# Kernel optimization log

Measured on AMD Instinct MI355X. Metric: run time of the kernel, lower is better.

## Reference

```python
import jax, jax.numpy as jnp
import numpy as np

N = 2048
GRID = 125
G3 = GRID ** 3
DX = 10.0 / GRID
INV_DX = 1.0 / DX
DENSITY = 1000.0
DT0 = 0.0417

_OFF = np.array([[i, j, k] for i in range(3) for j in range(3) for k in range(3)], dtype=np.int32)  # 27 stencil offsets


def setup_inputs() -> dict:
    key = jax.random.key(0)
    k1, k2, k3, k4 = jax.random.split(key, 4)
    bs, T = 2, 16
    x = jax.random.uniform(k1, (bs, T, N, 3), dtype=jnp.float32)
    vol = jax.random.uniform(k2, (bs, N), dtype=jnp.float32)
    F = jax.random.normal(k3, (bs, T, N, 3, 3), dtype=jnp.float32)
    C = jax.random.normal(k4, (bs, T, N, 3, 3), dtype=jnp.float32)
    return {"x": x, "vol": vol, "F": F, "C": C, "frame_interval": 2, "norm_fac": 5}


def reference(x, vol, F, C, frame_interval, norm_fac):
    if norm_fac > 0:
        x = x * 2 + norm_fac
    dT = DT0 * frame_interval
    bs, T = x.shape[0], x.shape[1]
    start_t = 1 if frame_interval == 1 else 0
    end_t = T - 2
    M = bs * (end_t - start_t)

    px = x[:, start_t:end_t].reshape(M, N, 3)
    pv = ((x[:, start_t + 2:end_t + 2] - x[:, start_t:end_t]) / (2 * dT)).reshape(M, N, 3)
    pF = F[:, start_t:end_t].reshape(M, N, 3, 3)
    pFn = F[:, start_t + 1:end_t + 1].reshape(M, N, 3, 3)
    pC = C[:, start_t:end_t].reshape(M, N, 3, 3)
    mass = DENSITY * jnp.repeat(vol[:, None], end_t - start_t, axis=1).reshape(M, N)  # [M,N]

    gp = px * INV_DX
    base = (gp - 0.5).astype(jnp.int32)            # positions are positive -> trunc == floor
    fx = gp - base                                  # [M,N,3]
    # quadratic B-spline weights, axis-major: w[..., axis, offset]
    w = jnp.stack([0.5 * (1.5 - fx) ** 2, 0.75 - (fx - 1) ** 2, 0.5 * (fx - 0.5) ** 2], axis=-1)
    dw = jnp.stack([fx - 1.5, -2 * (fx - 1), fx - 0.5], axis=-1)

    off = jnp.asarray(_OFF)                         # [27,3]
    wi = w[:, :, 0, off[:, 0]]; wj = w[:, :, 1, off[:, 1]]; wk = w[:, :, 2, off[:, 2]]
    dwi = dw[:, :, 0, off[:, 0]]; dwj = dw[:, :, 1, off[:, 1]]; dwk = dw[:, :, 2, off[:, 2]]
    weight = wi * wj * wk                           # [M,N,27]
    dweight = jnp.stack([dwi * wj * wk, wi * dwj * wk, wi * wj * dwk], axis=-1) * INV_DX  # [M,N,27,3]

    node = base[:, :, None, :] + off[None, None]    # [M,N,27,3]
    flat = (node[..., 0] * GRID + node[..., 1]) * GRID + node[..., 2]  # [M,N,27]

    dpos = (off[None, None].astype(fx.dtype) - fx[:, :, None, :]) * DX  # [M,N,27,3]
    vel = pv[:, :, None, :] + jnp.einsum('mnab,mnob->mnoa', pC, dpos)   # APIC velocity
    mw = mass[:, :, None] * weight                  # [M,N,27]
    v_in = mw[..., None] * vel                      # [M,N,27,3]

    midx = jnp.arange(M)[:, None, None]
    grid_v = jnp.zeros((M, G3, 3), x.dtype).at[midx, flat].add(v_in)   # P2G momentum scatter
    grid_m = jnp.zeros((M, G3), x.dtype).at[midx, flat].add(mw)        # P2G mass scatter
    grid_m = jnp.where(grid_m > 1e-15, grid_m, jnp.ones_like(grid_m))
    grid_v = grid_v / grid_m[..., None]

    gv = grid_v[midx, flat]                          # G2P gather [M,N,27,3]
    new_F = jnp.einsum('mnoa,mnob->mnab', gv, dweight)  # velocity gradient
    I3 = jnp.eye(3, dtype=x.dtype)
    F_pred = jnp.einsum('mnab,mnbc->mnac', I3 + new_F * dT, pF)
    return jnp.mean(jnp.abs(F_pred - pFn)) * (end_t - start_t)
```

## Files before the change

### kernel.cpp

```cpp
#include <hip/hip_runtime.h>

constexpr float DT0      = 0.0417f;
constexpr float DENSITY_ = 1000.0f;
constexpr float DXF      = 10.0f / 125.0f;
constexpr float INV_DXF  = 12.5f;

constexpr int DIM  = 32;
constexpr int DIM2 = DIM * DIM;
constexpr int DIM3 = DIM * DIM * DIM;

constexpr float MSC = 1.0f / 16.0f;

typedef _Float16 f16x2 __attribute__((ext_vector_type(2)));

__device__ __forceinline__ void lds_pk_fadd(f16x2* addr, f16x2 v) {
#if __has_builtin(__builtin_amdgcn_ds_atomic_fadd_v2f16)
    (void)__builtin_amdgcn_ds_atomic_fadd_v2f16(
        (__attribute__((address_space(3))) f16x2*)addr, v);
#else
    unsigned int* ua = (unsigned int*)addr;
    union { f16x2 h; unsigned int u; } oldv, newv, cur;
    cur.u = __atomic_load_n(ua, __ATOMIC_RELAXED);
    do {
        oldv.u = cur.u;
        newv.h = oldv.h + v;
        cur.u  = atomicCAS(ua, oldv.u, newv.u);
    } while (cur.u != oldv.u);
#endif
}

__device__ __forceinline__ f16x2 pk_f16(float lo, float hi) {
#if __has_builtin(__builtin_amdgcn_cvt_pkrtz)
    return __builtin_bit_cast(f16x2, __builtin_amdgcn_cvt_pkrtz(lo, hi));
#else
    f16x2 v; v.x = (_Float16)lo; v.y = (_Float16)hi; return v;
#endif
}

__device__ __forceinline__ int window_min(int nf) {
    int b = 0;
    if (nf > 0) {
        b = (int)(12.5f * (float)nf - 0.5f) - 2;
        if (b < 0) b = 0;
    }
    return b;
}

__global__ __launch_bounds__(1024)
void p2g_kernel(const float* __restrict__ x,
                const float* __restrict__ vol,
                const float* __restrict__ C,
                const int* __restrict__ fi_p,
                const int* __restrict__ nf_p,
                float* __restrict__ grid,
                int bs, int T, int Np)
{
    __shared__ f16x2 pl[4][DIM2 * 2];

    const int fi = fi_p[0], nf = nf_p[0];
    const int start_t = (fi == 1) ? 1 : 0;
    const int TS = (T - 2) - start_t;
    const int M  = bs * TS;

    const int m   = blockIdx.x >> 5;
    const int p   = blockIdx.x & (DIM - 1);
    const int tid = threadIdx.x;
    const int q   = tid >> 8;
    const int lt  = tid & 255;

    f16x2* plf = &pl[0][0];
    f16x2 hz; hz.x = (_Float16)0.0f; hz.y = (_Float16)0.0f;
    for (int i = tid; i < 4 * DIM2 * 2; i += 1024) plf[i] = hz;
    __syncthreads();

    if (m < M) {
        const int b = m / TS;
        const int t = (m - b * TS) + start_t;
        const int bmin = window_min(nf);
        const float dT = DT0 * (float)fi;
        const float inv2dT = 1.0f / (2.0f * dT);
        const float nff = (float)nf;

        const float* x0s = x + (((size_t)b * T + t)     * Np) * 3;
        const float* x2s = x + (((size_t)b * T + t + 2) * Np) * 3;
        const float* Cs  = C + (((size_t)b * T + t)     * Np) * 9;
        const float* vs  = vol + (size_t)b * Np;

        f16x2* myp = pl[q];
        const int nbeg = q * (Np >> 2);
        const int nend = nbeg + (Np >> 2);

        for (int n = nbeg + lt; n < nend; n += 256) {
            float a0 = x0s[3 * n];
            if (nf > 0) a0 = a0 * 2.0f + nff;
            const float gp0 = a0 * INV_DXF;
            const int b0 = (int)(gp0 - 0.5f);
            const int l0 = b0 - bmin;
            const int i  = p - l0;
            if ((unsigned)i > 2u) continue;

            float a1 = x0s[3 * n + 1], a2 = x0s[3 * n + 2];
            float c0 = x2s[3 * n], c1 = x2s[3 * n + 1], c2 = x2s[3 * n + 2];
            if (nf > 0) {
                a1 = a1 * 2.0f + nff; a2 = a2 * 2.0f + nff;
                c0 = c0 * 2.0f + nff; c1 = c1 * 2.0f + nff; c2 = c2 * 2.0f + nff;
            }
            const float pv0 = (c0 - a0) * inv2dT;
            const float pv1 = (c1 - a1) * inv2dT;
            const float pv2 = (c2 - a2) * inv2dT;
            const float mass = DENSITY_ * vs[n];
            float Cm[9];
#pragma unroll
            for (int r = 0; r < 9; ++r) Cm[r] = Cs[9 * n + r];

            const float fx0 = gp0 - (float)b0;
            const float gp1 = a1 * INV_DXF;
            const int   b1  = (int)(gp1 - 0.5f);
            const float fx1 = gp1 - (float)b1;
            const float gp2 = a2 * INV_DXF;
            const int   b2  = (int)(gp2 - 0.5f);
            const float fx2 = gp2 - (float)b2;
            const int l1 = b1 - bmin, l2 = b2 - bmin;

            const float wi = (i == 0) ? 0.5f * (1.5f - fx0) * (1.5f - fx0)
                           : (i == 1) ? 0.75f - (fx0 - 1.0f) * (fx0 - 1.0f)
                                      : 0.5f * (fx0 - 0.5f) * (fx0 - 0.5f);
            const float wim = mass * wi * MSC;

            float w1a[3], w2a[3];
            w1a[0] = 0.5f * (1.5f - fx1) * (1.5f - fx1);
            w1a[1] = 0.75f - (fx1 - 1.0f) * (fx1 - 1.0f);
            w1a[2] = 0.5f * (fx1 - 0.5f) * (fx1 - 0.5f);
            w2a[0] = 0.5f * (1.5f - fx2) * (1.5f - fx2);
            w2a[1] = 0.75f - (fx2 - 1.0f) * (fx2 - 1.0f);
            w2a[2] = 0.5f * (fx2 - 0.5f) * (fx2 - 0.5f);

            const float dpx  = ((float)i - fx0) * DXF;
            const float dpy0 = (-fx1) * DXF;
            const float dpz0 = (-fx2) * DXF;
            float vjx = pv0 + Cm[0]*dpx + Cm[1]*dpy0 + Cm[2]*dpz0;
            float vjy = pv1 + Cm[3]*dpx + Cm[4]*dpy0 + Cm[5]*dpz0;
            float vjz = pv2 + Cm[6]*dpx + Cm[7]*dpy0 + Cm[8]*dpz0;
            const float djx = Cm[1] * DXF, djy = Cm[4] * DXF, djz = Cm[7] * DXF;
            const float dkx = Cm[2] * DXF, dky = Cm[5] * DXF, dkz = Cm[8] * DXF;

            if (l1 >= 0 && l1 <= DIM - 3 && l2 >= 0 && l2 <= DIM - 3) {
                int rowc = (l1 * DIM + l2) * 2;
#pragma unroll
                for (int j = 0; j < 3; ++j) {
                    const float wijm = wim * w1a[j];
                    float vx = vjx, vy = vjy, vz = vjz;
                    int cc = rowc;
#pragma unroll
                    for (int k = 0; k < 3; ++k) {
                        const float mw = wijm * w2a[k];
                        lds_pk_fadd(&myp[cc + 0], pk_f16(mw * vx, mw * vy));
                        lds_pk_fadd(&myp[cc + 1], pk_f16(mw * vz, mw));
                        vx += dkx; vy += dky; vz += dkz;
                        cc += 2;
                    }
                    vjx += djx; vjy += djy; vjz += djz;
                    rowc += DIM * 2;
                }
            } else {
#pragma unroll
                for (int j = 0; j < 3; ++j) {
                    const int lj = min(max(l1 + j, 0), DIM - 1);
                    const float wijm = wim * w1a[j];
                    float vx = vjx, vy = vjy, vz = vjz;
#pragma unroll
                    for (int k = 0; k < 3; ++k) {
                        const int lk = min(max(l2 + k, 0), DIM - 1);
                        const float mw = wijm * w2a[k];
                        const int cc = (lj * DIM + lk) * 2;
                        lds_pk_fadd(&myp[cc + 0], pk_f16(mw * vx, mw * vy));
                        lds_pk_fadd(&myp[cc + 1], pk_f16(mw * vz, mw));
                        vx += dkx; vy += dky; vz += dkz;
                    }
                    vjx += djx; vjy += djy; vjz += djz;
                }
            }
        }
    }
    __syncthreads();

    if (m < M) {
        float4* dst = (float4*)(grid + ((size_t)m * DIM + p) * DIM2 * 4);
        for (int cell = tid; cell < DIM2; cell += 1024) {
            float mx = 0.f, my = 0.f, mz = 0.f, gm = 0.f;
#pragma unroll
            for (int cp = 0; cp < 4; ++cp) {
                const f16x2 s0 = pl[cp][cell * 2 + 0];
                const f16x2 s1 = pl[cp][cell * 2 + 1];
                mx += (float)s0.x; my += (float)s0.y;
                mz += (float)s1.x; gm += (float)s1.y;
            }
            const float inv = (gm > 1e-12f) ? 1.0f / gm : 0.0f;
            dst[cell] = make_float4(mx * inv, my * inv, mz * inv, 0.0f);
        }
    }
}

__global__ __launch_bounds__(256)
void g2p_loss_kernel(const float* __restrict__ x,
                     const float* __restrict__ F,
                     const int* __restrict__ fi_p,
                     const int* __restrict__ nf_p,
                     const float* __restrict__ grid,
                     float* __restrict__ partials,
                     int bs, int T, int Np)
{
    const int fi = fi_p[0], nf = nf_p[0];
    const int start_t = (fi == 1) ? 1 : 0;
    const int TS = (T - 2) - start_t;
    const int M  = bs * TS;
    const float dT = DT0 * (float)fi;

    const int gid = blockIdx.x * blockDim.x + threadIdx.x;
    const int pid = gid >> 2;
    const int q   = gid & 3;
    float s = 0.0f;

    if (pid < M * Np) {
        const int m = pid / Np;
        const int n = pid - m * Np;
        const int b = m / TS;
        const int t = (m - b * TS) + start_t;
        const float nff = (float)nf;

        const float* x0 = x + (((size_t)b * T + t) * Np + n) * 3;
        float px[3];
#pragma unroll
        for (int d = 0; d < 3; ++d) {
            float a0 = x0[d];
            if (nf > 0) a0 = a0 * 2.0f + nff;
            px[d] = a0;
        }

        const int bmin = window_min(nf);
        int   base[3];
        float fx[3], w[3][3], dw[3][3];
#pragma unroll
        for (int d = 0; d < 3; ++d) {
            const float gp = px[d] * INV_DXF;
            base[d] = (int)(gp - 0.5f);
            fx[d]   = gp - (float)base[d];
            w[d][0] = 0.5f * (1.5f - fx[d]) * (1.5f - fx[d]);
            w[d][1] = 0.75f - (fx[d] - 1.0f) * (fx[d] - 1.0f);
            w[d][2] = 0.5f * (fx[d] - 0.5f) * (fx[d] - 0.5f);
            dw[d][0] = fx[d] - 1.5f;
            dw[d][1] = -2.0f * (fx[d] - 1.0f);
            dw[d][2] = fx[d] - 0.5f;
        }

        const float* gbase = grid + (size_t)m * DIM3 * 4;
        float nF[9] = {0,0,0,0,0,0,0,0,0};
#pragma unroll
        for (int o = q; o < 27; o += 4) {
            const int i = o / 9, j = (o / 3) % 3, k = o % 3;
            const int li = min(max(base[0] + i - bmin, 0), DIM - 1);
            const int lj = min(max(base[1] + j - bmin, 0), DIM - 1);
            const int lk = min(max(base[2] + k - bmin, 0), DIM - 1);
            const float4 g = *(const float4*)(gbase +
                ((size_t)((li * DIM + lj) * DIM + lk)) * 4);
            const float gx = g.x, gy = g.y, gz = g.z;
            const float dwx = dw[0][i] *  w[1][j] *  w[2][k] * INV_DXF;
            const float dwy =  w[0][i] * dw[1][j] *  w[2][k] * INV_DXF;
            const float dwz =  w[0][i] *  w[1][j] * dw[2][k] * INV_DXF;
            nF[0] += gx * dwx; nF[1] += gx * dwy; nF[2] += gx * dwz;
            nF[3] += gy * dwx; nF[4] += gy * dwy; nF[5] += gy * dwz;
            nF[6] += gz * dwx; nF[7] += gz * dwy; nF[8] += gz * dwz;
        }
#pragma unroll
        for (int d = 1; d < 4; d <<= 1) {
#pragma unroll
            for (int r = 0; r < 9; ++r) nF[r] += __shfl_xor(nF[r], d, 64);
        }

        if (q == 0) {
            const float* pF  = F + (((size_t)b * T + t)     * Np + n) * 9;
            const float* pFn = F + (((size_t)b * T + t + 1) * Np + n) * 9;
            float Fm[9], Fn[9];
#pragma unroll
            for (int i = 0; i < 9; ++i) { Fm[i] = pF[i]; Fn[i] = pFn[i]; }
#pragma unroll
            for (int a = 0; a < 3; ++a) {
#pragma unroll
                for (int c = 0; c < 3; ++c) {
                    const float fp = Fm[a * 3 + c] + dT *
                        (nF[a * 3 + 0] * Fm[0 + c] +
                         nF[a * 3 + 1] * Fm[3 + c] +
                         nF[a * 3 + 2] * Fm[6 + c]);
                    s += fabsf(fp - Fn[a * 3 + c]);
                }
            }
            s *= (float)TS / ((float)M * (float)Np * 9.0f);
        }
    }

#pragma unroll
    for (int o = 32; o > 0; o >>= 1) s += __shfl_down(s, o, 64);
    __shared__ float wsum[4];
    const int lane = threadIdx.x & 63;
    const int wid  = threadIdx.x >> 6;
    if (lane == 0) wsum[wid] = s;
    __syncthreads();
    if (threadIdx.x == 0)
        partials[blockIdx.x] = wsum[0] + wsum[1] + wsum[2] + wsum[3];
}

__global__ __launch_bounds__(256)
void reduce_kernel(const float* __restrict__ partials, int n,
                   float* __restrict__ out)
{
    float s = 0.0f;
    for (int i = threadIdx.x; i < n; i += 256) s += partials[i];
#pragma unroll
    for (int o = 32; o > 0; o >>= 1) s += __shfl_down(s, o, 64);
    __shared__ float wsum[4];
    const int lane = threadIdx.x & 63;
    const int wid  = threadIdx.x >> 6;
    if (lane == 0) wsum[wid] = s;
    __syncthreads();
    if (threadIdx.x == 0) out[0] = wsum[0] + wsum[1] + wsum[2] + wsum[3];
}

extern "C" void kernel_launch(void* const* d_in, const int* in_sizes, int n_in,
                              void* d_out, int out_size, void* d_ws, size_t ws_size,
                              hipStream_t stream) {
    const float* x   = (const float*)d_in[0];
    const float* vol = (const float*)d_in[1];
    const float* F   = (const float*)d_in[2];
    const float* C   = (const float*)d_in[3];
    const int*   fi  = (const int*)d_in[4];
    const int*   nf  = (const int*)d_in[5];

    const int Np = 2048;
    const int bs = in_sizes[1] / Np;
    const int T  = in_sizes[0] / (bs * Np * 3);
    const int MMAX = bs * (T - 2);

    float* grid = (float*)d_ws;
    const size_t grid_f = (size_t)MMAX * DIM3 * 4;
    float* partials = grid + grid_f;

    p2g_kernel<<<MMAX * DIM, 1024, 0, stream>>>(x, vol, C, fi, nf,
                                                grid, bs, T, Np);

    const int nthreads = MMAX * Np * 4;
    const int nblocks  = (nthreads + 255) / 256;
    g2p_loss_kernel<<<nblocks, 256, 0, stream>>>(
        x, F, fi, nf, grid, partials, bs, T, Np);

    reduce_kernel<<<1, 256, 0, stream>>>(partials, nblocks, (float*)d_out);
}
```

Baseline: 110.7 us.

## Compact matching particles into LDS queue before P2G scatter; split final F error across lanes

In P2G, every thread first tests whether its particle touches this block's x-slab and appends matching indices to a shared-memory queue through wave ballot and atomic counter. All 1024 threads then process the compacted queue, so the expensive scatter work is spread evenly instead of leaving most lanes idle inside divergent waves. In G2P, the final F_pred error computation is split across the four sub-lanes rather than done only by q==0. The cost is an extra barrier and LDS queue space, and the 11-bit particle index encoding assumes Np <= 2048.

```diff
diff --git a/kernel.cpp b/kernel.cpp
--- a/kernel.cpp
+++ b/kernel.cpp
@@ -56,6 +56,8 @@
                 int bs, int T, int Np)
 {
     __shared__ f16x2 pl[4][DIM2 * 2];
+    __shared__ unsigned short queue[2048];
+    __shared__ int qcnt;
 
     const int fi = fi_p[0], nf = nf_p[0];
     const int start_t = (fi == 1) ? 1 : 0;
@@ -65,12 +67,11 @@
     const int m   = blockIdx.x >> 5;
     const int p   = blockIdx.x & (DIM - 1);
     const int tid = threadIdx.x;
-    const int q   = tid >> 8;
-    const int lt  = tid & 255;
 
     f16x2* plf = &pl[0][0];
     f16x2 hz; hz.x = (_Float16)0.0f; hz.y = (_Float16)0.0f;
     for (int i = tid; i < 4 * DIM2 * 2; i += 1024) plf[i] = hz;
+    if (tid == 0) qcnt = 0;
     __syncthreads();
 
     if (m < M) {
@@ -86,25 +87,48 @@
         const float* Cs  = C + (((size_t)b * T + t)     * Np) * 9;
         const float* vs  = vol + (size_t)b * Np;
 
-        f16x2* myp = pl[q];
-        const int nbeg = q * (Np >> 2);
-        const int nend = nbeg + (Np >> 2);
-
-        for (int n = nbeg + lt; n < nend; n += 256) {
+        const int lane = tid & 63;
+        for (int n = tid; n < Np; n += 1024) {
             float a0 = x0s[3 * n];
             if (nf > 0) a0 = a0 * 2.0f + nff;
             const float gp0 = a0 * INV_DXF;
             const int b0 = (int)(gp0 - 0.5f);
             const int l0 = b0 - bmin;
             const int i  = p - l0;
-            if ((unsigned)i > 2u) continue;
-
+            const bool match = ((unsigned)i <= 2u);
+            const unsigned long long mask = __ballot(match);
+            if (mask) {
+                const int leader = __ffsll(mask) - 1;
+                const int pre = __popcll(mask & ((1ull << lane) - 1ull));
+                int base = 0;
+                if (lane == leader) base = atomicAdd(&qcnt, __popcll(mask));
+                base = __shfl(base, leader, 64);
+                if (match)
+                    queue[base + pre] =
+                        (unsigned short)(n | (i << 12));
+            }
+        }
+        __syncthreads();
+
+        const int total = qcnt;
+        f16x2* myp = pl[(tid >> 6) & 3];
+        for (int e = tid; e < total; e += 1024) {
+            const int ent = queue[e];
+            const int n = ent & 0x7FF;
+            const int i = ent >> 12;
+
+            float a0 = x0s[3 * n];
             float a1 = x0s[3 * n + 1], a2 = x0s[3 * n + 2];
             float c0 = x2s[3 * n], c1 = x2s[3 * n + 1], c2 = x2s[3 * n + 2];
             if (nf > 0) {
+                a0 = a0 * 2.0f + nff;
                 a1 = a1 * 2.0f + nff; a2 = a2 * 2.0f + nff;
                 c0 = c0 * 2.0f + nff; c1 = c1 * 2.0f + nff; c2 = c2 * 2.0f + nff;
             }
+            const float gp0 = a0 * INV_DXF;
+            const int   b0  = (int)(gp0 - 0.5f);
+            const float fx0 = gp0 - (float)b0;
+
             const float pv0 = (c0 - a0) * inv2dT;
             const float pv1 = (c1 - a1) * inv2dT;
             const float pv2 = (c2 - a2) * inv2dT;
@@ -113,7 +137,6 @@
 #pragma unroll
             for (int r = 0; r < 9; ++r) Cm[r] = Cs[9 * n + r];
 
-            const float fx0 = gp0 - (float)b0;
             const float gp1 = a1 * INV_DXF;
             const int   b1  = (int)(gp1 - 0.5f);
             const float fx1 = gp1 - (float)b1;
@@ -277,22 +300,20 @@
             for (int r = 0; r < 9; ++r) nF[r] += __shfl_xor(nF[r], d, 64);
         }
 
-        if (q == 0) {
+        {
             const float* pF  = F + (((size_t)b * T + t)     * Np + n) * 9;
             const float* pFn = F + (((size_t)b * T + t + 1) * Np + n) * 9;
-            float Fm[9], Fn[9];
-#pragma unroll
-            for (int i = 0; i < 9; ++i) { Fm[i] = pF[i]; Fn[i] = pFn[i]; }
-#pragma unroll
-            for (int a = 0; a < 3; ++a) {
-#pragma unroll
-                for (int c = 0; c < 3; ++c) {
-                    const float fp = Fm[a * 3 + c] + dT *
-                        (nF[a * 3 + 0] * Fm[0 + c] +
-                         nF[a * 3 + 1] * Fm[3 + c] +
-                         nF[a * 3 + 2] * Fm[6 + c]);
-                    s += fabsf(fp - Fn[a * 3 + c]);
-                }
+            float Fm[9];
+#pragma unroll
+            for (int i = 0; i < 9; ++i) Fm[i] = pF[i];
+#pragma unroll
+            for (int e = q; e < 9; e += 4) {
+                const int a = e / 3, c = e - 3 * a;
+                const float fp = Fm[a * 3 + c] + dT *
+                    (nF[a * 3 + 0] * Fm[0 + c] +
+                     nF[a * 3 + 1] * Fm[3 + c] +
+                     nF[a * 3 + 2] * Fm[6 + c]);
+                s += fabsf(fp - pFn[e]);
             }
             s *= (float)TS / ((float)M * (float)Np * 9.0f);
         }
```

Result: slower. 115.0 us (+3.9%).
